# Performance work log

Measured on AMD Instinct MI355X. Metric: run time of the kernel, lower is better.

The kernel has to match this reference:

```python
import jax, jax.numpy as jnp
import numpy as np

COLDNESS = 1.0
ITERATION = 10


def setup_inputs() -> dict:
    key = jax.random.key(0)
    k1, k2 = jax.random.split(key)
    B, N, T = 16, 8, 65536
    inp = jax.random.normal(k1, (B, N, T), dtype=jnp.float32)
    tgt = jax.random.normal(k2, (B, N, T), dtype=jnp.float32)
    return {"input": inp, "target": tgt}


def reference(input, target):
    # Pairwise MSE criterion: loss[b, i, j] = mean_t (input[b,i,t] - target[b,j,t])^2
    diff = input[:, :, None, :] - target[:, None, :, :]        # [B, N, N, T]
    possible_loss = jnp.mean(diff * diff, axis=-1)             # [B, N, N]

    # Sinkhorn-Knopp normalization in log space
    Z = -COLDNESS * possible_loss
    for _ in range(ITERATION):
        Z = Z - jax.nn.logsumexp(Z, axis=1, keepdims=True)
        Z = Z - jax.nn.logsumexp(Z, axis=2, keepdims=True)

    permutation_matrix = jnp.exp(Z)                            # [B, N, N]
    loss = jnp.sum((possible_loss + Z / COLDNESS) * permutation_matrix, axis=(1, 2))
    loss = jnp.mean(loss)                                      # batch_mean=True
    pattern = jnp.argmax(permutation_matrix, axis=2)           # [B, N]
    return loss, pattern
```

## Files before the change

kernel.cpp:

```cpp
#include <hip/hip_runtime.h>
#include <hip/hip_bf16.h>


#define BATCH 16
#define NROW 8
#define TLEN 65536
#define CHUNKS 32
#define THREADS 256

__global__ __launch_bounds__(THREADS)
void sinkpit_dist_kernel(const float* __restrict__ x,
                         const float* __restrict__ y,
                         float* __restrict__ ws) {
    const int b     = blockIdx.y;
    const int chunk = blockIdx.x;
    const int tid   = threadIdx.x;
    const int lane  = tid & 63;
    const int wave  = tid >> 6;

    const float* xb = x + (size_t)b * NROW * TLEN;
    const float* yb = y + (size_t)b * NROW * TLEN;
    const int base = chunk * (TLEN / CHUNKS);

    float a[64];
    #pragma unroll
    for (int c = 0; c < 64; ++c) a[c] = 0.0f;

    #pragma unroll
    for (int k = 0; k < 2; ++k) {
        const int t0 = base + (k * THREADS + tid) * 4;
        float4 xv[8], yv[8];
        #pragma unroll
        for (int i = 0; i < 8; ++i)
            xv[i] = *(const float4*)(xb + (size_t)i * TLEN + t0);
        #pragma unroll
        for (int j = 0; j < 8; ++j)
            yv[j] = *(const float4*)(yb + (size_t)j * TLEN + t0);
        #pragma unroll
        for (int i = 0; i < 8; ++i) {
            #pragma unroll
            for (int j = 0; j < 8; ++j) {
                float d0 = xv[i].x - yv[j].x;
                float d1 = xv[i].y - yv[j].y;
                float d2 = xv[i].z - yv[j].z;
                float d3 = xv[i].w - yv[j].w;
                a[i * 8 + j] += d0 * d0 + d1 * d1 + d2 * d2 + d3 * d3;
            }
        }
    }

    #pragma unroll
    for (int o = 32; o >= 1; o >>= 1) {
        const bool up = (lane & o) != 0;
        #pragma unroll
        for (int c = 0; c < o; ++c) {
            float send = up ? a[c] : a[c + o];
            float recv = __shfl_xor(send, o);
            float keep = up ? a[c + o] : a[c];
            a[c] = keep + recv;
        }
    }

    __shared__ float red[4][64];
    red[wave][lane] = a[0];
    __syncthreads();
    if (tid < 64) {
        float v = red[0][tid] + red[1][tid] + red[2][tid] + red[3][tid];
        atomicAdd(&ws[b * 64 + tid], v);
    }
}

__global__ __launch_bounds__(1024)
void sinkpit_sinkhorn_kernel(const float* __restrict__ ws,
                             float* __restrict__ out) {
    const int tid  = threadIdx.x;
    const int b    = tid >> 6;
    const int lane = tid & 63;
    const int i    = lane >> 3;
    const int j    = lane & 7;

    const float S = ws[b * 64 + lane] * (1.0f / (float)TLEN);
    float Z = -S;

    for (int it = 0; it < 10; ++it) {
        float m = Z;
        m = fmaxf(m, __shfl_xor(m, 8));
        m = fmaxf(m, __shfl_xor(m, 16));
        m = fmaxf(m, __shfl_xor(m, 32));
        float e = expf(Z - m);
        e += __shfl_xor(e, 8);
        e += __shfl_xor(e, 16);
        e += __shfl_xor(e, 32);
        Z -= m + logf(e);
        m = Z;
        m = fmaxf(m, __shfl_xor(m, 1));
        m = fmaxf(m, __shfl_xor(m, 2));
        m = fmaxf(m, __shfl_xor(m, 4));
        e = expf(Z - m);
        e += __shfl_xor(e, 1);
        e += __shfl_xor(e, 2);
        e += __shfl_xor(e, 4);
        Z -= m + logf(e);
    }

    const float P = expf(Z);
    float contrib = (S + Z) * P;

    float tot = contrib;
    tot += __shfl_xor(tot, 32);
    tot += __shfl_xor(tot, 16);
    tot += __shfl_xor(tot, 8);
    tot += __shfl_xor(tot, 4);
    tot += __shfl_xor(tot, 2);
    tot += __shfl_xor(tot, 1);

    __shared__ float lossred[BATCH];
    if (lane == 0) lossred[b] = tot;

    float v = Z;
    int   idx = j;
    {
        float ov; int oi;
        ov = __shfl_xor(v, 1); oi = __shfl_xor(idx, 1);
        if (ov > v || (ov == v && oi < idx)) { v = ov; idx = oi; }
        ov = __shfl_xor(v, 2); oi = __shfl_xor(idx, 2);
        if (ov > v || (ov == v && oi < idx)) { v = ov; idx = oi; }
        ov = __shfl_xor(v, 4); oi = __shfl_xor(idx, 4);
        if (ov > v || (ov == v && oi < idx)) { v = ov; idx = oi; }
    }
    if (j == 0) out[1 + b * NROW + i] = (float)idx;

    __syncthreads();
    if (tid == 0) {
        float L = 0.0f;
        #pragma unroll
        for (int bb = 0; bb < BATCH; ++bb) L += lossred[bb];
        out[0] = L * (1.0f / (float)BATCH);
    }
}

extern "C" void kernel_launch(void* const* d_in, const int* in_sizes, int n_in,
                              void* d_out, int out_size, void* d_ws, size_t ws_size,
                              hipStream_t stream) {
    const float* inp = (const float*)d_in[0];
    const float* tgt = (const float*)d_in[1];
    float* out = (float*)d_out;
    float* ws  = (float*)d_ws;

    hipMemsetAsync(ws, 0, BATCH * 64 * sizeof(float), stream);

    dim3 grid(CHUNKS, BATCH);
    sinkpit_dist_kernel<<<grid, THREADS, 0, stream>>>(inp, tgt, ws);
    sinkpit_sinkhorn_kernel<<<1, BATCH * 64, 0, stream>>>(ws, out);
}
```

Measured before the change: 105.4 us.

## Replace atomic accumulation with per-chunk partials, double chunks, use fast exp/log

```diff
diff --git a/kernel.cpp b/kernel.cpp
--- a/kernel.cpp
+++ b/kernel.cpp
@@ -5,7 +5,7 @@
 #define BATCH 16
 #define NROW 8
 #define TLEN 65536
-#define CHUNKS 32
+#define CHUNKS 64
 #define THREADS 256
 
 __global__ __launch_bounds__(THREADS)
@@ -20,32 +20,25 @@
 
     const float* xb = x + (size_t)b * NROW * TLEN;
     const float* yb = y + (size_t)b * NROW * TLEN;
-    const int base = chunk * (TLEN / CHUNKS);
+    const int t0 = chunk * (TLEN / CHUNKS) + tid * 4;
 
     float a[64];
+
+    float4 yv[8];
     #pragma unroll
-    for (int c = 0; c < 64; ++c) a[c] = 0.0f;
+    for (int j = 0; j < 8; ++j)
+        yv[j] = *(const float4*)(yb + (size_t)j * TLEN + t0);
 
     #pragma unroll
-    for (int k = 0; k < 2; ++k) {
-        const int t0 = base + (k * THREADS + tid) * 4;
-        float4 xv[8], yv[8];
+    for (int i = 0; i < 8; ++i) {
+        const float4 xv = *(const float4*)(xb + (size_t)i * TLEN + t0);
         #pragma unroll
-        for (int i = 0; i < 8; ++i)
-            xv[i] = *(const float4*)(xb + (size_t)i * TLEN + t0);
-        #pragma unroll
-        for (int j = 0; j < 8; ++j)
-            yv[j] = *(const float4*)(yb + (size_t)j * TLEN + t0);
-        #pragma unroll
-        for (int i = 0; i < 8; ++i) {
-            #pragma unroll
-            for (int j = 0; j < 8; ++j) {
-                float d0 = xv[i].x - yv[j].x;
-                float d1 = xv[i].y - yv[j].y;
-                float d2 = xv[i].z - yv[j].z;
-                float d3 = xv[i].w - yv[j].w;
-                a[i * 8 + j] += d0 * d0 + d1 * d1 + d2 * d2 + d3 * d3;
-            }
+        for (int j = 0; j < 8; ++j) {
+            float d0 = xv.x - yv[j].x;
+            float d1 = xv.y - yv[j].y;
+            float d2 = xv.z - yv[j].z;
+            float d3 = xv.w - yv[j].w;
+            a[i * 8 + j] = d0 * d0 + d1 * d1 + d2 * d2 + d3 * d3;
         }
     }
 
@@ -66,7 +59,7 @@
     __syncthreads();
     if (tid < 64) {
         float v = red[0][tid] + red[1][tid] + red[2][tid] + red[3][tid];
-        atomicAdd(&ws[b * 64 + tid], v);
+        ws[((size_t)b * CHUNKS + chunk) * 64 + tid] = v;
     }
 }
 
@@ -79,7 +72,12 @@
     const int i    = lane >> 3;
     const int j    = lane & 7;
 
-    const float S = ws[b * 64 + lane] * (1.0f / (float)TLEN);
+    float ssum = 0.0f;
+    #pragma unroll 8
+    for (int c = 0; c < CHUNKS; ++c)
+        ssum += ws[((size_t)b * CHUNKS + c) * 64 + lane];
+
+    const float S = ssum * (1.0f / (float)TLEN);
     float Z = -S;
 
     for (int it = 0; it < 10; ++it) {
@@ -87,23 +85,23 @@
         m = fmaxf(m, __shfl_xor(m, 8));
         m = fmaxf(m, __shfl_xor(m, 16));
         m = fmaxf(m, __shfl_xor(m, 32));
-        float e = expf(Z - m);
+        float e = __expf(Z - m);
         e += __shfl_xor(e, 8);
         e += __shfl_xor(e, 16);
         e += __shfl_xor(e, 32);
-        Z -= m + logf(e);
+        Z -= m + __logf(e);
         m = Z;
         m = fmaxf(m, __shfl_xor(m, 1));
         m = fmaxf(m, __shfl_xor(m, 2));
         m = fmaxf(m, __shfl_xor(m, 4));
-        e = expf(Z - m);
+        e = __expf(Z - m);
         e += __shfl_xor(e, 1);
         e += __shfl_xor(e, 2);
         e += __shfl_xor(e, 4);
-        Z -= m + logf(e);
+        Z -= m + __logf(e);
     }
 
-    const float P = expf(Z);
+    const float P = __expf(Z);
     float contrib = (S + Z) * P;
 
     float tot = contrib;
@@ -147,8 +145,6 @@
     float* out = (float*)d_out;
     float* ws  = (float*)d_ws;
 
-    hipMemsetAsync(ws, 0, BATCH * 64 * sizeof(float), stream);
-
     dim3 grid(CHUNKS, BATCH);
     sinkpit_dist_kernel<<<grid, THREADS, 0, stream>>>(inp, tgt, ws);
     sinkpit_sinkhorn_kernel<<<1, BATCH * 64, 0, stream>>>(ws, out);
```

After: 103.5 us. About the same (-1.9%).
